# Optimization experiments

Hardware: AMD Instinct MI355X
Metric: run time of the kernel (lower is better)

Reference implementation:

```python
import jax, jax.numpy as jnp
import numpy as np

DIM = 1024
HEADS = 8
DIM_HEAD = 64
HIDDEN = HEADS * DIM_HEAD  # 512
SCALE = DIM_HEAD ** -0.5
BATCH = 16384
EPS = 1e-12  # F.normalize eps


def setup_inputs() -> dict:
    key = jax.random.key(0)
    k0, k1, k2 = jax.random.split(key, 3)
    x = jax.random.normal(k0, (BATCH, DIM), dtype=jnp.float32)
    w_qkv = jax.random.normal(k1, (3 * HIDDEN, DIM), dtype=jnp.float32) * 0.02
    w_out = jax.random.normal(k2, (DIM, HIDDEN), dtype=jnp.float32) * 0.02
    b_out = jnp.zeros((DIM,), dtype=jnp.float32)
    g = jnp.ones((1, DIM), dtype=jnp.float32)
    return {"x": x, "w_qkv": w_qkv, "w_out": w_out, "b_out": b_out, "g": g}


def reference(x, w_qkv, w_out, b_out, g):
    b = x.shape[0]
    # Conv1d(kernel=1, no bias) on n=1 sequence == matmul with (3*hidden, dim) weight
    qkv = x @ w_qkv.T  # (b, 3*hidden)
    q, k, v = jnp.split(qkv, 3, axis=1)  # each (b, hidden)
    # rearrange 'b (h c) n -> b h c n' with n=1 -> (b, h, c)
    q = q.reshape(b, HEADS, DIM_HEAD)
    k = k.reshape(b, HEADS, DIM_HEAD)
    v = v.reshape(b, HEADS, DIM_HEAD)
    # q.softmax(dim=-2) is over the c axis
    q = jax.nn.softmax(q, axis=-1) * SCALE
    # k.softmax(dim=-1) is over the n axis of size 1 -> all ones (kept faithful)
    k = jax.nn.softmax(k[..., None], axis=-1)[..., 0]
    # context = einsum('bhdn,bhen->bhde', k, v); out = einsum('bhde,bhdn->bhen', context, q)
    # with n=1 this collapses to out_e = (sum_d k_d q_d) * v_e; fused to avoid (b,h,d,e)
    s = jnp.einsum('bhd,bhd->bh', k, q)  # (b, h)
    out = s[..., None] * v  # (b, h, e)
    out = out.reshape(b, HIDDEN)  # 'b h c n -> b (h c) n', squeeze(-1)
    # Linear(hidden, dim)
    out = out @ w_out.T + b_out  # (b, dim)
    # RMSNorm_MLP: F.normalize(x, dim=1) * g * sqrt(dim)
    norm = jnp.linalg.norm(out, axis=1, keepdims=True)
    out = out / jnp.maximum(norm, EPS) * g * jnp.sqrt(jnp.float32(DIM))
    return out
```

## Files before the change

kernel.cpp:

```cpp
#include <hip/hip_runtime.h>
#include <hip/hip_bf16.h>


typedef __attribute__((ext_vector_type(8))) short bf16x8;
typedef __attribute__((ext_vector_type(4))) float f32x4;

struct alignas(16) bfvec8 { __hip_bfloat16 h[8]; };

__device__ __forceinline__ bfvec8 pack8(float4 a, float4 b) {
    bfvec8 o;
    o.h[0] = __float2bfloat16(a.x); o.h[1] = __float2bfloat16(a.y);
    o.h[2] = __float2bfloat16(a.z); o.h[3] = __float2bfloat16(a.w);
    o.h[4] = __float2bfloat16(b.x); o.h[5] = __float2bfloat16(b.y);
    o.h[6] = __float2bfloat16(b.z); o.h[7] = __float2bfloat16(b.w);
    return o;
}

__global__ __launch_bounds__(256)
void cast_bf16(const float* __restrict__ in, bfvec8* __restrict__ out, int n8) {
    int i = blockIdx.x * blockDim.x + threadIdx.x;
    if (i >= n8) return;
    const float4* p = (const float4*)in + (size_t)i * 2;
    out[i] = pack8(p[0], p[1]);
}

__global__ __launch_bounds__(256)
void weff_fused(const float* __restrict__ Wo, const float* __restrict__ Wv,
                __hip_bfloat16* __restrict__ Weff) {
    __shared__ __align__(16) __hip_bfloat16 As[128 * 32];
    __shared__ __align__(16) __hip_bfloat16 Bs[128 * 32];
    __shared__ __align__(16) float Bf[32 * 132];

    const int tid  = threadIdx.x;
    const int lane = tid & 63;
    const int wave = tid >> 6;
    const int wm   = wave >> 1;
    const int wn   = wave & 1;
    const int quad = lane >> 4;
    const int tr   = lane & 15;
    const int m0   = blockIdx.y * 128;
    const int n0   = blockIdx.x * 128;

    f32x4 acc[4][4];
#pragma unroll
    for (int i = 0; i < 4; ++i)
#pragma unroll
        for (int j = 0; j < 4; ++j)
            acc[i][j] = (f32x4){0.f, 0.f, 0.f, 0.f};

    for (int kt = 0; kt < 512; kt += 32) {
#pragma unroll
        for (int i = 0; i < 2; ++i) {
            int L = i * 256 + tid;
            int r = L >> 2, c8 = (L & 3) << 3;
            const float* s = Wo + (size_t)(m0 + r) * 512 + kt + c8;
            float4 a = *(const float4*)s, b = *(const float4*)(s + 4);
            *(bfvec8*)(As + r * 32 + c8) = pack8(a, b);
        }
#pragma unroll
        for (int i = 0; i < 2; ++i) {
            int L = i * 256 + tid;
            int kr = L >> 4, c8 = (L & 15) << 3;
            const float* s = Wv + (size_t)(kt + kr) * 1024 + n0 + c8;
            float4 a = *(const float4*)s, b = *(const float4*)(s + 4);
            *(float4*)(Bf + kr * 132 + c8)     = a;
            *(float4*)(Bf + kr * 132 + c8 + 4) = b;
        }
        __syncthreads();
#pragma unroll
        for (int i = 0; i < 2; ++i) {
            int L = i * 256 + tid;
            int n = L >> 2, k8 = (L & 3) << 3;
            float4 a, b;
            a.x = Bf[(k8 + 0) * 132 + n]; a.y = Bf[(k8 + 1) * 132 + n];
            a.z = Bf[(k8 + 2) * 132 + n]; a.w = Bf[(k8 + 3) * 132 + n];
            b.x = Bf[(k8 + 4) * 132 + n]; b.y = Bf[(k8 + 5) * 132 + n];
            b.z = Bf[(k8 + 6) * 132 + n]; b.w = Bf[(k8 + 7) * 132 + n];
            *(bfvec8*)(Bs + n * 32 + k8) = pack8(a, b);
        }
        __syncthreads();

        bf16x8 af[4], bf[4];
#pragma unroll
        for (int mi = 0; mi < 4; ++mi)
            af[mi] = *(const bf16x8*)(As + ((wm * 64 + mi * 16 + tr) * 32 + quad * 8));
#pragma unroll
        for (int ni = 0; ni < 4; ++ni)
            bf[ni] = *(const bf16x8*)(Bs + ((wn * 64 + ni * 16 + tr) * 32 + quad * 8));
#pragma unroll
        for (int mi = 0; mi < 4; ++mi)
#pragma unroll
            for (int ni = 0; ni < 4; ++ni)
                acc[mi][ni] = __builtin_amdgcn_mfma_f32_16x16x32_bf16(
                    af[mi], bf[ni], acc[mi][ni], 0, 0, 0);
        __syncthreads();
    }

#pragma unroll
    for (int mi = 0; mi < 4; ++mi)
#pragma unroll
        for (int ni = 0; ni < 4; ++ni) {
            const int col = n0 + wn * 64 + ni * 16 + tr;
#pragma unroll
            for (int r = 0; r < 4; ++r) {
                const int row = m0 + wm * 64 + mi * 16 + quad * 4 + r;
                Weff[(size_t)row * 1024 + col] =
                    __float2bfloat16(acc[mi][ni][r] * 0.125f);
            }
        }
}

__global__ __launch_bounds__(256)
void main_gemm(const __hip_bfloat16* __restrict__ A,
               const __hip_bfloat16* __restrict__ Bt,
               const float* __restrict__ bias,
               __hip_bfloat16* __restrict__ Y) {
    __shared__ __align__(16) __hip_bfloat16 As[128 * 64];
    __shared__ __align__(16) __hip_bfloat16 Bs[128 * 64];

    const int tid  = threadIdx.x;
    const int lane = tid & 63;
    const int wave = tid >> 6;
    const int wm   = wave >> 1;
    const int wn   = wave & 1;
    const int quad = lane >> 4;
    const int tr   = lane & 15;

    const int b   = blockIdx.x;
    const int xcd = b & 7;
    const int t   = b >> 3;
    const int nt  = t & 7;
    const int mt  = (t >> 3) * 8 + xcd;
    const int m0  = mt * 128;
    const int n0  = nt * 128;

    f32x4 acc[4][4];
#pragma unroll
    for (int i = 0; i < 4; ++i)
#pragma unroll
        for (int j = 0; j < 4; ++j)
            acc[i][j] = (f32x4){0.f, 0.f, 0.f, 0.f};

    for (int kt = 0; kt < 1024; kt += 64) {
#pragma unroll
        for (int i = 0; i < 4; ++i) {
            int L = i * 256 + tid;
            int r = L >> 3;
            int c = L & 7;
            int kg = (c ^ (r & 7)) << 3;
            const __hip_bfloat16* ga = A  + (size_t)(m0 + r) * 1024 + kt + kg;
            const __hip_bfloat16* gb = Bt + (size_t)(n0 + r) * 1024 + kt + kg;
            __builtin_amdgcn_global_load_lds(
                (const __attribute__((address_space(1))) void*)ga,
                (__attribute__((address_space(3))) void*)(As + (size_t)L * 8), 16, 0, 0);
            __builtin_amdgcn_global_load_lds(
                (const __attribute__((address_space(1))) void*)gb,
                (__attribute__((address_space(3))) void*)(Bs + (size_t)L * 8), 16, 0, 0);
        }
        __syncthreads();

#pragma unroll
        for (int ko = 0; ko < 2; ++ko) {
            bf16x8 af[4], bf[4];
#pragma unroll
            for (int mi = 0; mi < 4; ++mi) {
                int r = wm * 64 + mi * 16 + tr;
                int c = (ko * 4 + quad) ^ (r & 7);
                af[mi] = *(const bf16x8*)(As + (r * 8 + c) * 8);
            }
#pragma unroll
            for (int ni = 0; ni < 4; ++ni) {
                int r = wn * 64 + ni * 16 + tr;
                int c = (ko * 4 + quad) ^ (r & 7);
                bf[ni] = *(const bf16x8*)(Bs + (r * 8 + c) * 8);
            }
#pragma unroll
            for (int mi = 0; mi < 4; ++mi)
#pragma unroll
                for (int ni = 0; ni < 4; ++ni)
                    acc[mi][ni] = __builtin_amdgcn_mfma_f32_16x16x32_bf16(
                        af[mi], bf[ni], acc[mi][ni], 0, 0, 0);
        }
        __syncthreads();
    }

#pragma unroll
    for (int mi = 0; mi < 4; ++mi)
#pragma unroll
        for (int ni = 0; ni < 4; ++ni) {
            const int col = n0 + wn * 64 + ni * 16 + tr;
            const float bv = bias[col];
#pragma unroll
            for (int r = 0; r < 4; ++r) {
                const int row = m0 + wm * 64 + mi * 16 + quad * 4 + r;
                Y[(size_t)row * 1024 + col] = __float2bfloat16(acc[mi][ni][r] + bv);
            }
        }
}

__global__ __launch_bounds__(256)
void rmsnorm2(const __hip_bfloat16* __restrict__ y, const float* __restrict__ g,
              float* __restrict__ out) {
    const int wave = threadIdx.x >> 6;
    const int sub  = wave >> 1;
    const int t    = threadIdx.x & 127;
    const int row  = blockIdx.x * 2 + sub;
    const size_t base = (size_t)row * 1024 + t * 8;

    union { uint4 u; ushort s[8]; } U;
    U.u = *(const uint4*)(y + base);
    float v[8];
#pragma unroll
    for (int j = 0; j < 8; ++j)
        v[j] = __bfloat162float(*(const __hip_bfloat16*)&U.s[j]);

    float ss = 0.f;
#pragma unroll
    for (int j = 0; j < 8; ++j) ss += v[j] * v[j];
#pragma unroll
    for (int off = 32; off > 0; off >>= 1)
        ss += __shfl_down(ss, off, 64);

    __shared__ float wsum[4];
    if ((threadIdx.x & 63) == 0) wsum[wave] = ss;
    __syncthreads();
    const float total = wsum[sub * 2] + wsum[sub * 2 + 1];
    const float sc = 32.0f / fmaxf(sqrtf(total), 1e-12f);

    const float4 g0 = *(const float4*)(g + t * 8);
    const float4 g1 = *(const float4*)(g + t * 8 + 4);
    float4 o0, o1;
    o0.x = v[0] * sc * g0.x; o0.y = v[1] * sc * g0.y;
    o0.z = v[2] * sc * g0.z; o0.w = v[3] * sc * g0.w;
    o1.x = v[4] * sc * g1.x; o1.y = v[5] * sc * g1.y;
    o1.z = v[6] * sc * g1.z; o1.w = v[7] * sc * g1.w;
    *(float4*)(out + base)     = o0;
    *(float4*)(out + base + 4) = o1;
}

extern "C" void kernel_launch(void* const* d_in, const int* in_sizes, int n_in,
                              void* d_out, int out_size, void* d_ws, size_t ws_size,
                              hipStream_t stream) {
    const float* x     = (const float*)d_in[0];
    const float* w_qkv = (const float*)d_in[1];
    const float* w_out = (const float*)d_in[2];
    const float* b_out = (const float*)d_in[3];
    const float* g     = (const float*)d_in[4];

    const int B = 16384, D = 1024, H = 512;
    const float* wv = w_qkv + (size_t)2 * H * D;

    char* ws = (char*)d_ws;
    size_t off = 0;
    __hip_bfloat16* x_bf    = (__hip_bfloat16*)(ws + off); off += (size_t)B * D * 2;
    __hip_bfloat16* weff_bf = (__hip_bfloat16*)(ws + off); off += (size_t)D * D * 2;
    __hip_bfloat16* y_bf    = (__hip_bfloat16*)(ws + off); off += (size_t)B * D * 2;

    cast_bf16<<<(B * D / 8) / 256, 256, 0, stream>>>(x, (bfvec8*)x_bf, B * D / 8);
    weff_fused<<<dim3(8, 8), 256, 0, stream>>>(w_out, wv, weff_bf);
    main_gemm<<<1024, 256, 0, stream>>>(x_bf, weff_bf, b_out, y_bf);
    rmsnorm2<<<B / 2, 256, 0, stream>>>(y_bf, g, (float*)d_out);
}
```

Baseline: 203.2 us.

## Fuse x fp32-to-bf16 cast into main GEMM and shrink Weff tiles

Removes the separate cast_bf16 kernel. The main GEMM now reads fp32 x directly, holds the next k-tile in registers as a software prefetch, and converts to bf16 while storing to LDS. The weff_fused kernel moves to 64x64 tiles (256 blocks instead of 64) with an XOR swizzle to spread the small precompute over more CUs. The fused path drops one full pass over x through memory, but each A tile in the GEMM now loads twice as many bytes and uses more registers. Since there are 8 column tiles, each A tile is cast to bf16 eight times instead of once.

```diff
diff --git a/kernel.cpp b/kernel.cpp
--- a/kernel.cpp
+++ b/kernel.cpp
@@ -17,19 +17,11 @@
 }
 
 __global__ __launch_bounds__(256)
-void cast_bf16(const float* __restrict__ in, bfvec8* __restrict__ out, int n8) {
-    int i = blockIdx.x * blockDim.x + threadIdx.x;
-    if (i >= n8) return;
-    const float4* p = (const float4*)in + (size_t)i * 2;
-    out[i] = pack8(p[0], p[1]);
-}
-
-__global__ __launch_bounds__(256)
 void weff_fused(const float* __restrict__ Wo, const float* __restrict__ Wv,
                 __hip_bfloat16* __restrict__ Weff) {
-    __shared__ __align__(16) __hip_bfloat16 As[128 * 32];
-    __shared__ __align__(16) __hip_bfloat16 Bs[128 * 32];
-    __shared__ __align__(16) float Bf[32 * 132];
+    __shared__ __align__(16) __hip_bfloat16 As[64 * 32];
+    __shared__ __align__(16) __hip_bfloat16 Bs[64 * 32];
+    __shared__ __align__(16) float Bf[32 * 65];
 
     const int tid  = threadIdx.x;
     const int lane = tid & 63;
@@ -38,72 +30,75 @@
     const int wn   = wave & 1;
     const int quad = lane >> 4;
     const int tr   = lane & 15;
-    const int m0   = blockIdx.y * 128;
-    const int n0   = blockIdx.x * 128;
-
-    f32x4 acc[4][4];
-#pragma unroll
-    for (int i = 0; i < 4; ++i)
-#pragma unroll
-        for (int j = 0; j < 4; ++j)
+    const int m0   = blockIdx.y * 64;
+    const int n0   = blockIdx.x * 64;
+
+    f32x4 acc[2][2];
+#pragma unroll
+    for (int i = 0; i < 2; ++i)
+#pragma unroll
+        for (int j = 0; j < 2; ++j)
             acc[i][j] = (f32x4){0.f, 0.f, 0.f, 0.f};
 
     for (int kt = 0; kt < 512; kt += 32) {
-#pragma unroll
-        for (int i = 0; i < 2; ++i) {
-            int L = i * 256 + tid;
-            int r = L >> 2, c8 = (L & 3) << 3;
-            const float* s = Wo + (size_t)(m0 + r) * 512 + kt + c8;
-            float4 a = *(const float4*)s, b = *(const float4*)(s + 4);
-            *(bfvec8*)(As + r * 32 + c8) = pack8(a, b);
-        }
-#pragma unroll
-        for (int i = 0; i < 2; ++i) {
-            int L = i * 256 + tid;
-            int kr = L >> 4, c8 = (L & 15) << 3;
-            const float* s = Wv + (size_t)(kt + kr) * 1024 + n0 + c8;
-            float4 a = *(const float4*)s, b = *(const float4*)(s + 4);
-            *(float4*)(Bf + kr * 132 + c8)     = a;
-            *(float4*)(Bf + kr * 132 + c8 + 4) = b;
-        }
-        __syncthreads();
-#pragma unroll
-        for (int i = 0; i < 2; ++i) {
-            int L = i * 256 + tid;
-            int n = L >> 2, k8 = (L & 3) << 3;
+        {
+            int r = tid >> 2, c = tid & 3;
+            int s = (r >> 1) & 3;
+            int kg = (c ^ s) << 3;
+            const float* sp = Wo + (size_t)(m0 + r) * 512 + kt + kg;
+            float4 a = *(const float4*)sp, b = *(const float4*)(sp + 4);
+            *(bfvec8*)(As + r * 32 + (c << 3)) = pack8(a, b);
+        }
+        {
+            int kr = tid >> 3, c8 = (tid & 7) << 3;
+            const float* sp = Wv + (size_t)(kt + kr) * 1024 + n0 + c8;
+            float4 a = *(const float4*)sp, b = *(const float4*)(sp + 4);
+            *(float4*)(Bf + kr * 65 + c8)     = a;
+            *(float4*)(Bf + kr * 65 + c8 + 4) = b;
+        }
+        __syncthreads();
+        {
+            int n = tid >> 2, cc = tid & 3, k8 = cc << 3;
             float4 a, b;
-            a.x = Bf[(k8 + 0) * 132 + n]; a.y = Bf[(k8 + 1) * 132 + n];
-            a.z = Bf[(k8 + 2) * 132 + n]; a.w = Bf[(k8 + 3) * 132 + n];
-            b.x = Bf[(k8 + 4) * 132 + n]; b.y = Bf[(k8 + 5) * 132 + n];
-            b.z = Bf[(k8 + 6) * 132 + n]; b.w = Bf[(k8 + 7) * 132 + n];
-            *(bfvec8*)(Bs + n * 32 + k8) = pack8(a, b);
-        }
-        __syncthreads();
-
-        bf16x8 af[4], bf[4];
-#pragma unroll
-        for (int mi = 0; mi < 4; ++mi)
-            af[mi] = *(const bf16x8*)(As + ((wm * 64 + mi * 16 + tr) * 32 + quad * 8));
-#pragma unroll
-        for (int ni = 0; ni < 4; ++ni)
-            bf[ni] = *(const bf16x8*)(Bs + ((wn * 64 + ni * 16 + tr) * 32 + quad * 8));
-#pragma unroll
-        for (int mi = 0; mi < 4; ++mi)
-#pragma unroll
-            for (int ni = 0; ni < 4; ++ni)
+            a.x = Bf[(k8 + 0) * 65 + n]; a.y = Bf[(k8 + 1) * 65 + n];
+            a.z = Bf[(k8 + 2) * 65 + n]; a.w = Bf[(k8 + 3) * 65 + n];
+            b.x = Bf[(k8 + 4) * 65 + n]; b.y = Bf[(k8 + 5) * 65 + n];
+            b.z = Bf[(k8 + 6) * 65 + n]; b.w = Bf[(k8 + 7) * 65 + n];
+            int cs = cc ^ ((n >> 1) & 3);
+            *(bfvec8*)(Bs + n * 32 + cs * 8) = pack8(a, b);
+        }
+        __syncthreads();
+
+        bf16x8 af[2], bf[2];
+#pragma unroll
+        for (int mi = 0; mi < 2; ++mi) {
+            int r = wm * 32 + mi * 16 + tr;
+            int c = quad ^ ((r >> 1) & 3);
+            af[mi] = *(const bf16x8*)(As + r * 32 + c * 8);
+        }
+#pragma unroll
+        for (int ni = 0; ni < 2; ++ni) {
+            int r = wn * 32 + ni * 16 + tr;
+            int c = quad ^ ((r >> 1) & 3);
+            bf[ni] = *(const bf16x8*)(Bs + r * 32 + c * 8);
+        }
+#pragma unroll
+        for (int mi = 0; mi < 2; ++mi)
+#pragma unroll
+            for (int ni = 0; ni < 2; ++ni)
                 acc[mi][ni] = __builtin_amdgcn_mfma_f32_16x16x32_bf16(
                     af[mi], bf[ni], acc[mi][ni], 0, 0, 0);
         __syncthreads();
     }
 
 #pragma unroll
-    for (int mi = 0; mi < 4; ++mi)
-#pragma unroll
-        for (int ni = 0; ni < 4; ++ni) {
-            const int col = n0 + wn * 64 + ni * 16 + tr;
+    for (int mi = 0; mi < 2; ++mi)
+#pragma unroll
+        for (int ni = 0; ni < 2; ++ni) {
+            const int col = n0 + wn * 32 + ni * 16 + tr;
 #pragma unroll
             for (int r = 0; r < 4; ++r) {
-                const int row = m0 + wm * 64 + mi * 16 + quad * 4 + r;
+                const int row = m0 + wm * 32 + mi * 16 + quad * 4 + r;
                 Weff[(size_t)row * 1024 + col] =
                     __float2bfloat16(acc[mi][ni][r] * 0.125f);
             }
@@ -111,7 +106,7 @@
 }
 
 __global__ __launch_bounds__(256)
-void main_gemm(const __hip_bfloat16* __restrict__ A,
+void main_gemm(const float* __restrict__ X,
                const __hip_bfloat16* __restrict__ Bt,
                const float* __restrict__ bias,
                __hip_bfloat16* __restrict__ Y) {
@@ -134,6 +129,17 @@
     const int m0  = mt * 128;
     const int n0  = nt * 128;
 
+    int rr[4], kgg[4];
+    size_t abase[4];
+#pragma unroll
+    for (int i = 0; i < 4; ++i) {
+        int L = i * 256 + tid;
+        rr[i]  = L >> 3;
+        int c  = L & 7;
+        kgg[i] = (c ^ (rr[i] & 7)) << 3;
+        abase[i] = (size_t)(m0 + rr[i]) * 1024 + kgg[i];
+    }
+
     f32x4 acc[4][4];
 #pragma unroll
     for (int i = 0; i < 4; ++i)
@@ -141,23 +147,38 @@
         for (int j = 0; j < 4; ++j)
             acc[i][j] = (f32x4){0.f, 0.f, 0.f, 0.f};
 
+    float4 pa[4], pb[4];
+#pragma unroll
+    for (int i = 0; i < 4; ++i) {
+        const float* s = X + abase[i];
+        pa[i] = *(const float4*)s;
+        pb[i] = *(const float4*)(s + 4);
+    }
+
     for (int kt = 0; kt < 1024; kt += 64) {
 #pragma unroll
         for (int i = 0; i < 4; ++i) {
             int L = i * 256 + tid;
-            int r = L >> 3;
-            int c = L & 7;
-            int kg = (c ^ (r & 7)) << 3;
-            const __hip_bfloat16* ga = A  + (size_t)(m0 + r) * 1024 + kt + kg;
-            const __hip_bfloat16* gb = Bt + (size_t)(n0 + r) * 1024 + kt + kg;
-            __builtin_amdgcn_global_load_lds(
-                (const __attribute__((address_space(1))) void*)ga,
-                (__attribute__((address_space(3))) void*)(As + (size_t)L * 8), 16, 0, 0);
+            const __hip_bfloat16* gb = Bt + (size_t)(n0 + rr[i]) * 1024 + kt + kgg[i];
             __builtin_amdgcn_global_load_lds(
                 (const __attribute__((address_space(1))) void*)gb,
                 (__attribute__((address_space(3))) void*)(Bs + (size_t)L * 8), 16, 0, 0);
         }
-        __syncthreads();
+#pragma unroll
+        for (int i = 0; i < 4; ++i) {
+            int L = i * 256 + tid;
+            *(bfvec8*)(As + (size_t)L * 8) = pack8(pa[i], pb[i]);
+        }
+        __syncthreads();
+
+        if (kt + 64 < 1024) {
+#pragma unroll
+            for (int i = 0; i < 4; ++i) {
+                const float* s = X + abase[i] + kt + 64;
+                pa[i] = *(const float4*)s;
+                pb[i] = *(const float4*)(s + 4);
+            }
+        }
 
 #pragma unroll
         for (int ko = 0; ko < 2; ++ko) {
@@ -252,12 +273,10 @@
 
     char* ws = (char*)d_ws;
     size_t off = 0;
-    __hip_bfloat16* x_bf    = (__hip_bfloat16*)(ws + off); off += (size_t)B * D * 2;
     __hip_bfloat16* weff_bf = (__hip_bfloat16*)(ws + off); off += (size_t)D * D * 2;
     __hip_bfloat16* y_bf    = (__hip_bfloat16*)(ws + off); off += (size_t)B * D * 2;
 
-    cast_bf16<<<(B * D / 8) / 256, 256, 0, stream>>>(x, (bfvec8*)x_bf, B * D / 8);
-    weff_fused<<<dim3(8, 8), 256, 0, stream>>>(w_out, wv, weff_bf);
-    main_gemm<<<1024, 256, 0, stream>>>(x_bf, weff_bf, b_out, y_bf);
+    weff_fused<<<dim3(D / 64, D / 64), 256, 0, stream>>>(w_out, wv, weff_bf);
+    main_gemm<<<1024, 256, 0, stream>>>(x, weff_bf, b_out, y_bf);
     rmsnorm2<<<B / 2, 256, 0, stream>>>(y_bf, g, (float*)d_out);
 }
```

After: 193.0 us. 1.05x faster.
